# Kernel optimization log

Measured on AMD Instinct MI355X. Metric: run time of the kernel, lower is better.

The kernel has to match this reference:

```python
import jax, jax.numpy as jnp
import numpy as np

B = 524288      # batch
D = 16          # ds_dim
N = 32          # number of dynamical systems
H = 128         # gating hidden width


def setup_inputs() -> dict:
    key = jax.random.key(0)
    ks = jax.random.split(key, 8)
    x_cur = jax.random.normal(ks[0], (B, D), dtype=jnp.float32)
    W1 = jax.random.normal(ks[1], (H, D), dtype=jnp.float32) * 0.1
    b1 = jax.random.normal(ks[2], (H,), dtype=jnp.float32) * 0.1
    W2 = jax.random.normal(ks[3], (N, H), dtype=jnp.float32) * 0.1
    b2 = jax.random.normal(ks[4], (N,), dtype=jnp.float32) * 0.1
    # B matrices are PSD (geotorch.positive_semidefinite), C are skew-symmetric (geotorch.skew)
    Braw = jax.random.normal(ks[5], (N, D, D), dtype=jnp.float32) * 0.3
    B_mats = jnp.einsum('nij,nkj->nik', Braw, Braw)  # PSD: R R^T
    Craw = jax.random.normal(ks[6], (N, D, D), dtype=jnp.float32) * 0.3
    C_mats = 0.5 * (Craw - jnp.swapaxes(Craw, -1, -2))  # skew-symmetric
    x_target = jax.random.normal(ks[7], (1, D), dtype=jnp.float32)
    return {"x_cur": x_cur, "W1": W1, "b1": b1, "W2": W2, "b2": b2,
            "B_mats": B_mats, "C_mats": C_mats, "x_target": x_target}


def reference(x_cur, W1, b1, W2, b2, B_mats, C_mats, x_target):
    # gating weights: softmax(Linear -> ReLU -> Linear)
    h = jax.nn.relu(x_cur @ W1.T + b1)          # [B, H]
    w_all = jax.nn.softmax(h @ W2.T + b2, axis=1)  # [B, N]
    # per-system linear map A_i = B_i + C_i applied to (x* - x)
    A = B_mats + C_mats                          # [N, D, D]
    diff = x_target - x_cur                      # [B, D]
    # torch.mm(A, diff.T).T == diff @ A.T -> proj[b,n,k] = sum_d A[n,k,d] diff[b,d]
    proj = jnp.einsum('nkd,bd->bnk', A, diff)    # [B, N, D]
    out = jnp.einsum('bn,bnk->bk', w_all, proj)  # [B, D]
    return out
```

## Files before the change

kernel.cpp:

```cpp
#include <hip/hip_runtime.h>

#define BATCH 524288

typedef __bf16 bf16x8 __attribute__((ext_vector_type(8)));
typedef __bf16 bf16x2 __attribute__((ext_vector_type(2)));
typedef float f32x4 __attribute__((ext_vector_type(4)));
typedef float f32x8 __attribute__((ext_vector_type(8)));
typedef float f32x2 __attribute__((ext_vector_type(2)));

#define SW1 16384
#define SZC 20480
#define SW2 20512
#define SB2 28704
#define SXT 28832
#define SB1 28896
#define SHC 29408
#define NWAVES 8
#define SMEM_BYTES (29408 + NWAVES * 2560)

__device__ __forceinline__ f32x8 load8(const float* __restrict__ p) {
    float4 a = *(const float4*)p;
    float4 b = *(const float4*)(p + 4);
    f32x8 v = {a.x, a.y, a.z, a.w, b.x, b.y, b.z, b.w};
    return v;
}

__device__ __forceinline__ int pack2bf(float a, float b) {
    f32x2 v = {a, b};
    bf16x2 p = __builtin_convertvector(v, bf16x2);
    return __builtin_bit_cast(int, p);
}

__global__ __launch_bounds__(512, 3) void andp_v13(
    const float* __restrict__ x_cur,
    const float* __restrict__ W1,
    const float* __restrict__ b1,
    const float* __restrict__ W2,
    const float* __restrict__ b2,
    const float* __restrict__ Bm,
    const float* __restrict__ Cm,
    const float* __restrict__ x_t,
    float* __restrict__ out)
{
    extern __shared__ char smem[];
    int* sA2i = (int*)smem;
    int* sW1i = (int*)(smem + SW1);
    int* sW2i = (int*)(smem + SW2);
    const int tid = threadIdx.x;

#pragma unroll
    for (int i = 0; i < 8; ++i) {
        int o2 = tid + i * 512;
        int o  = o2 * 2;
        int kk = o >> 9, qp = (o >> 7) & 3, k = (o >> 3) & 15, j = o & 7;
        int n = 2 * kk + (qp >> 1), d = (qp & 1) * 8 + j;
        int src = n * 256 + k * 16 + d;
        float2 bv = *(const float2*)(Bm + src);
        float2 cv = *(const float2*)(Cm + src);
        sA2i[o2] = pack2bf(bv.x + cv.x, bv.y + cv.y);
    }
#pragma unroll
    for (int i = 0; i < 2; ++i) {
        int o2 = tid + i * 512;
        int o  = o2 * 2;
        int t = o >> 8, qq = (o >> 7) & 1, cc = (o >> 3) & 15, j = o & 7;
        int src = (t * 16 + cc) * 16 + qq * 8 + j;
        float2 v = *(const float2*)(W1 + src);
        sW1i[o2] = pack2bf(v.x, v.y);
    }
    if (tid < 8) ((int*)(smem + SZC))[tid] = 0;
#pragma unroll
    for (int i = 0; i < 4; ++i) {
        int o2 = tid + i * 512;
        int chunk = o2 >> 8, rem = o2 & 255;
        int ln = rem >> 2, j2 = rem & 3;
        int qq = ln >> 4, cc = ln & 15;
        int t2 = chunk >> 2, s = chunk & 3;
        int src = (t2 * 16 + cc) * 128 + s * 32 + 4 * qq + j2;
        sW2i[o2] = pack2bf(W2[src], W2[src + 16]);
    }
    if (tid < 32) ((float*)(smem + SB2))[tid] = b2[tid];
    if (tid < 16) ((float*)(smem + SXT))[tid] = x_t[tid];
    if (tid < 128) ((float*)(smem + SB1))[tid] = b1[tid];

    const int wave = tid >> 6, lane = tid & 63;
    const int c = lane & 15, q = lane >> 4;
    const int qh = q >> 1;
    const int hh = (q & 1) * 8;
    const int c4 = c * 4;

    const char* sW1f = smem + SW1;
    const int w1base = (q < 2) ? ((q * 16 + c) * 16) : (SZC - SW1);
    const int w1step = (q < 2) ? 512 : 0;
    const char* sW2f = smem + SW2 + lane * 16;
    __bf16* hcw0 = (__bf16*)(smem + SHC + wave * 2560);
    __bf16* hcw1 = hcw0 + 640;
    const float* sB2f = (const float*)(smem + SB2);
    const float* sXTf = (const float*)(smem + SXT);
    const float* sB1f = (const float*)(smem + SB1);

    __syncthreads();

    const int blk_row = blockIdx.x * 512 + wave * 64;
    const f32x4 z4 = {0.f, 0.f, 0.f, 0.f};

#pragma unroll 1
    for (int p = 0; p < 2; ++p) {
        const int r0 = blk_row + p * 32;

        bf16x8 af[2];
#pragma unroll
        for (int t01 = 0; t01 < 2; ++t01) {
            f32x8 xv = load8(x_cur + (size_t)(r0 + t01 * 16 + c) * 16 + hh);
            af[t01] = __builtin_convertvector(xv, bf16x8);
        }

        f32x4 acc2[2][2];
        acc2[0][0] = z4; acc2[0][1] = z4; acc2[1][0] = z4; acc2[1][1] = z4;
#pragma unroll
        for (int s = 0; s < 4; ++s) {
            float b1a = sB1f[(2 * s) * 16 + c];
            float b1b = sB1f[(2 * s + 1) * 16 + c];
#pragma unroll
            for (int t01 = 0; t01 < 2; ++t01) {
                __bf16* hcw = t01 ? hcw1 : hcw0;
                bf16x8 w1a = *(const bf16x8*)(sW1f + w1base + (2 * s) * w1step);
                bf16x8 w1b = *(const bf16x8*)(sW1f + w1base + (2 * s + 1) * w1step);
                f32x4 a1a = __builtin_amdgcn_mfma_f32_16x16x32_bf16(af[t01], w1a, z4, 0, 0, 0);
                f32x4 a1b = __builtin_amdgcn_mfma_f32_16x16x32_bf16(af[t01], w1b, z4, 0, 0, 0);
#pragma unroll
                for (int r = 0; r < 4; ++r) {
                    float va = fmaxf(a1a[r] + b1a, 0.f);
                    float vb = fmaxf(a1b[r] + b1b, 0.f);
                    *(int*)(hcw + (q * 4 + r) * 40 + 2 * c) = pack2bf(va, vb);
                }
            }
#pragma unroll
            for (int t01 = 0; t01 < 2; ++t01) {
                __bf16* hcw = t01 ? hcw1 : hcw0;
                bf16x8 hb = *(const bf16x8*)(hcw + c * 40 + q * 8);
                bf16x8 w20 = *(const bf16x8*)(sW2f + (0 * 4 + s) * 1024);
                bf16x8 w21 = *(const bf16x8*)(sW2f + (1 * 4 + s) * 1024);
                acc2[t01][0] = __builtin_amdgcn_mfma_f32_16x16x32_bf16(w20, hb, acc2[t01][0], 0, 0, 0);
                acc2[t01][1] = __builtin_amdgcn_mfma_f32_16x16x32_bf16(w21, hb, acc2[t01][1], 0, 0, 0);
            }
        }

        int wq[8];
        {
            f32x4 bq0 = *(const f32x4*)(sB2f + q * 4);
            f32x4 bq1 = *(const f32x4*)(sB2f + 16 + q * 4);
#pragma unroll
            for (int t01 = 0; t01 < 2; ++t01) {
                float e[8], sum = 0.f;
#pragma unroll
                for (int r = 0; r < 4; ++r) {
                    e[r]     = __expf(acc2[t01][0][r] + bq0[r]);
                    e[4 + r] = __expf(acc2[t01][1][r] + bq1[r]);
                    sum += e[r] + e[4 + r];
                }
                sum += __shfl_xor(sum, 16, 64);
                sum += __shfl_xor(sum, 32, 64);
                float inv = 1.0f / sum;
                if (t01 == 0) {
#pragma unroll
                    for (int i = 0; i < 8; ++i) wq[i] = pack2bf(e[i] * inv, 0.f);
                } else {
#pragma unroll
                    for (int i = 0; i < 8; ++i) wq[i] |= pack2bf(0.f, e[i] * inv);
                }
            }
        }

        f32x8 dif[2];
        {
            f32x4 xta = *(const f32x4*)(sXTf + hh);
            f32x4 xtb = *(const f32x4*)(sXTf + hh + 4);
            f32x8 xtv = {xta[0], xta[1], xta[2], xta[3], xtb[0], xtb[1], xtb[2], xtb[3]};
            dif[0] = xtv - __builtin_convertvector(af[0], f32x8);
            dif[1] = xtv - __builtin_convertvector(af[1], f32x8);
        }

        f32x4 acc3[2];
        acc3[0] = z4; acc3[1] = z4;
#pragma unroll
        for (int kk = 0; kk < 16; ++kk) {
            const int lo = (kk >> 3) * 4 + 2 * (kk & 1);
            const int bpi = c4 + ((kk >> 1) & 3) * 64;
            int bpA = __builtin_amdgcn_ds_bpermute(bpi, wq[lo]);
            int bpB = __builtin_amdgcn_ds_bpermute(bpi, wq[lo + 1]);
            int sel = qh ? bpB : bpA;
            float w0 = __builtin_bit_cast(float, (unsigned)sel << 16);
            float w1 = __builtin_bit_cast(float, (unsigned)sel & 0xffff0000u);
            bf16x8 a2f = *(const bf16x8*)(smem + kk * 1024 + lane * 16);
            bf16x8 g0 = __builtin_convertvector(dif[0] * w0, bf16x8);
            bf16x8 g1 = __builtin_convertvector(dif[1] * w1, bf16x8);
            acc3[0] = __builtin_amdgcn_mfma_f32_16x16x32_bf16(a2f, g0, acc3[0], 0, 0, 0);
            acc3[1] = __builtin_amdgcn_mfma_f32_16x16x32_bf16(a2f, g1, acc3[1], 0, 0, 0);
        }

#pragma unroll
        for (int t01 = 0; t01 < 2; ++t01) {
            float4 st = make_float4(acc3[t01][0], acc3[t01][1], acc3[t01][2], acc3[t01][3]);
            *(float4*)(out + (size_t)(r0 + t01 * 16 + c) * 16 + q * 4) = st;
        }
    }
}

extern "C" void kernel_launch(void* const* d_in, const int* in_sizes, int n_in,
                              void* d_out, int out_size, void* d_ws, size_t ws_size,
                              hipStream_t stream) {
    const float* x_cur = (const float*)d_in[0];
    const float* W1    = (const float*)d_in[1];
    const float* b1    = (const float*)d_in[2];
    const float* W2    = (const float*)d_in[3];
    const float* b2    = (const float*)d_in[4];
    const float* Bm    = (const float*)d_in[5];
    const float* Cm    = (const float*)d_in[6];
    const float* x_t   = (const float*)d_in[7];
    float* out = (float*)d_out;

    const int blocks = BATCH / 512;
    andp_v13<<<blocks, 512, SMEM_BYTES, stream>>>(
        x_cur, W1, b1, W2, b2, Bm, Cm, x_t, out);
}
```

Baseline: 118.4 us.

## Fold biases into MFMA accumulators, prefetch next x tile, pack bf16 pairwise

Both biases now enter through the MFMA accumulator inputs: b1 is broadcast to float4 in shared memory and used as the initial C operand, and b2 is preloaded into acc2. This removes per-element bias adds before the ReLU and the exp. The x_cur rows for the second pass are loaded during the first pass so global latency overlaps compute. The gated diff is built with packed f32x2 multiplies and pairwise bf16 conversion. Shared memory grows slightly and register pressure rises from the prefetch.

```diff
diff --git a/kernel.cpp b/kernel.cpp
--- a/kernel.cpp
+++ b/kernel.cpp
@@ -7,6 +7,7 @@
 typedef float f32x4 __attribute__((ext_vector_type(4)));
 typedef float f32x8 __attribute__((ext_vector_type(8)));
 typedef float f32x2 __attribute__((ext_vector_type(2)));
+typedef int   i32x4 __attribute__((ext_vector_type(4)));
 
 #define SW1 16384
 #define SZC 20480
@@ -14,9 +15,9 @@
 #define SB2 28704
 #define SXT 28832
 #define SB1 28896
-#define SHC 29408
+#define SHC 30944
 #define NWAVES 8
-#define SMEM_BYTES (29408 + NWAVES * 2560)
+#define SMEM_BYTES (30944 + NWAVES * 2560)
 
 __device__ __forceinline__ f32x8 load8(const float* __restrict__ p) {
     float4 a = *(const float4*)p;
@@ -31,7 +32,7 @@
     return __builtin_bit_cast(int, p);
 }
 
-__global__ __launch_bounds__(512, 3) void andp_v13(
+__global__ __launch_bounds__(512, 3) void andp_v14(
     const float* __restrict__ x_cur,
     const float* __restrict__ W1,
     const float* __restrict__ b1,
@@ -81,7 +82,10 @@
     }
     if (tid < 32) ((float*)(smem + SB2))[tid] = b2[tid];
     if (tid < 16) ((float*)(smem + SXT))[tid] = x_t[tid];
-    if (tid < 128) ((float*)(smem + SB1))[tid] = b1[tid];
+    if (tid < 128) {
+        float v = b1[tid];
+        ((float4*)(smem + SB1))[tid] = make_float4(v, v, v, v);
+    }
 
     const int wave = tid >> 6, lane = tid & 63;
     const int c = lane & 15, q = lane >> 4;
@@ -97,41 +101,44 @@
     __bf16* hcw1 = hcw0 + 640;
     const float* sB2f = (const float*)(smem + SB2);
     const float* sXTf = (const float*)(smem + SXT);
-    const float* sB1f = (const float*)(smem + SB1);
+    const float* sB1r = (const float*)(smem + SB1);
 
     __syncthreads();
 
     const int blk_row = blockIdx.x * 512 + wave * 64;
     const f32x4 z4 = {0.f, 0.f, 0.f, 0.f};
+
+    const f32x4 bq0 = *(const f32x4*)(sB2f + q * 4);
+    const f32x4 bq1 = *(const f32x4*)(sB2f + 16 + q * 4);
+
+    bf16x8 af[2];
+#pragma unroll
+    for (int t01 = 0; t01 < 2; ++t01) {
+        f32x8 xv = load8(x_cur + (size_t)(blk_row + t01 * 16 + c) * 16 + hh);
+        af[t01] = __builtin_convertvector(xv, bf16x8);
+    }
 
 #pragma unroll 1
     for (int p = 0; p < 2; ++p) {
         const int r0 = blk_row + p * 32;
 
-        bf16x8 af[2];
-#pragma unroll
-        for (int t01 = 0; t01 < 2; ++t01) {
-            f32x8 xv = load8(x_cur + (size_t)(r0 + t01 * 16 + c) * 16 + hh);
-            af[t01] = __builtin_convertvector(xv, bf16x8);
-        }
-
         f32x4 acc2[2][2];
-        acc2[0][0] = z4; acc2[0][1] = z4; acc2[1][0] = z4; acc2[1][1] = z4;
+        acc2[0][0] = bq0; acc2[0][1] = bq1; acc2[1][0] = bq0; acc2[1][1] = bq1;
 #pragma unroll
         for (int s = 0; s < 4; ++s) {
-            float b1a = sB1f[(2 * s) * 16 + c];
-            float b1b = sB1f[(2 * s + 1) * 16 + c];
+            f32x4 cba = *(const f32x4*)(sB1r + ((2 * s) * 16 + c) * 4);
+            f32x4 cbb = *(const f32x4*)(sB1r + ((2 * s + 1) * 16 + c) * 4);
 #pragma unroll
             for (int t01 = 0; t01 < 2; ++t01) {
                 __bf16* hcw = t01 ? hcw1 : hcw0;
                 bf16x8 w1a = *(const bf16x8*)(sW1f + w1base + (2 * s) * w1step);
                 bf16x8 w1b = *(const bf16x8*)(sW1f + w1base + (2 * s + 1) * w1step);
-                f32x4 a1a = __builtin_amdgcn_mfma_f32_16x16x32_bf16(af[t01], w1a, z4, 0, 0, 0);
-                f32x4 a1b = __builtin_amdgcn_mfma_f32_16x16x32_bf16(af[t01], w1b, z4, 0, 0, 0);
+                f32x4 a1a = __builtin_amdgcn_mfma_f32_16x16x32_bf16(af[t01], w1a, cba, 0, 0, 0);
+                f32x4 a1b = __builtin_amdgcn_mfma_f32_16x16x32_bf16(af[t01], w1b, cbb, 0, 0, 0);
 #pragma unroll
                 for (int r = 0; r < 4; ++r) {
-                    float va = fmaxf(a1a[r] + b1a, 0.f);
-                    float vb = fmaxf(a1b[r] + b1b, 0.f);
+                    float va = fmaxf(a1a[r], 0.f);
+                    float vb = fmaxf(a1b[r], 0.f);
                     *(int*)(hcw + (q * 4 + r) * 40 + 2 * c) = pack2bf(va, vb);
                 }
             }
@@ -146,17 +153,23 @@
             }
         }
 
+        bf16x8 afn0 = af[0], afn1 = af[1];
+        if (p == 0) {
+            f32x8 xv0 = load8(x_cur + (size_t)(blk_row + 32 + c) * 16 + hh);
+            f32x8 xv1 = load8(x_cur + (size_t)(blk_row + 48 + c) * 16 + hh);
+            afn0 = __builtin_convertvector(xv0, bf16x8);
+            afn1 = __builtin_convertvector(xv1, bf16x8);
+        }
+
         int wq[8];
         {
-            f32x4 bq0 = *(const f32x4*)(sB2f + q * 4);
-            f32x4 bq1 = *(const f32x4*)(sB2f + 16 + q * 4);
 #pragma unroll
             for (int t01 = 0; t01 < 2; ++t01) {
                 float e[8], sum = 0.f;
 #pragma unroll
                 for (int r = 0; r < 4; ++r) {
-                    e[r]     = __expf(acc2[t01][0][r] + bq0[r]);
-                    e[4 + r] = __expf(acc2[t01][1][r] + bq1[r]);
+                    e[r]     = __expf(acc2[t01][0][r]);
+                    e[4 + r] = __expf(acc2[t01][1][r]);
                     sum += e[r] + e[4 + r];
                 }
                 sum += __shfl_xor(sum, 16, 64);
@@ -192,9 +205,20 @@
             int sel = qh ? bpB : bpA;
             float w0 = __builtin_bit_cast(float, (unsigned)sel << 16);
             float w1 = __builtin_bit_cast(float, (unsigned)sel & 0xffff0000u);
+            f32x2 w0p = {w0, w0}, w1p = {w1, w1};
+            i32x4 g0i, g1i;
+#pragma unroll
+            for (int jj = 0; jj < 4; ++jj) {
+                f32x2 d0 = {dif[0][2 * jj], dif[0][2 * jj + 1]};
+                f32x2 d1 = {dif[1][2 * jj], dif[1][2 * jj + 1]};
+                f32x2 p0 = d0 * w0p;
+                f32x2 p1 = d1 * w1p;
+                g0i[jj] = pack2bf(p0[0], p0[1]);
+                g1i[jj] = pack2bf(p1[0], p1[1]);
+            }
             bf16x8 a2f = *(const bf16x8*)(smem + kk * 1024 + lane * 16);
-            bf16x8 g0 = __builtin_convertvector(dif[0] * w0, bf16x8);
-            bf16x8 g1 = __builtin_convertvector(dif[1] * w1, bf16x8);
+            bf16x8 g0 = __builtin_bit_cast(bf16x8, g0i);
+            bf16x8 g1 = __builtin_bit_cast(bf16x8, g1i);
             acc3[0] = __builtin_amdgcn_mfma_f32_16x16x32_bf16(a2f, g0, acc3[0], 0, 0, 0);
             acc3[1] = __builtin_amdgcn_mfma_f32_16x16x32_bf16(a2f, g1, acc3[1], 0, 0, 0);
         }
@@ -204,6 +228,9 @@
             float4 st = make_float4(acc3[t01][0], acc3[t01][1], acc3[t01][2], acc3[t01][3]);
             *(float4*)(out + (size_t)(r0 + t01 * 16 + c) * 16 + q * 4) = st;
         }
+
+        af[0] = afn0;
+        af[1] = afn1;
     }
 }
 
@@ -221,6 +248,6 @@
     float* out = (float*)d_out;
 
     const int blocks = BATCH / 512;
-    andp_v13<<<blocks, 512, SMEM_BYTES, stream>>>(
+    andp_v14<<<blocks, 512, SMEM_BYTES, stream>>>(
         x_cur, W1, b1, W2, b2, Bm, Cm, x_t, out);
 }
```

After: 116.8 us. About the same (-1.4%).
